# Optimization experiments

Measured on AMD Instinct MI355X. Metric: run time of the kernel, lower is better.

The kernel has to match this reference:

```python
import jax, jax.numpy as jnp
import numpy as np

B, T, D, V = 64, 2048, 64, 100000


def create_beta_stack(feats, times):
    """feats: [F,B,T] float, times: [B,T] float.
    beta[:, :, i] = (times[:,i]-times[:,i-1] + mask_{i-1} * beta[:,:,i-1]) * (times[:,i] != -1)
    where mask = (feat != -1) & (feat != 0). Sequential reset/accumulate scan over T."""
    dt = times[:, 1:] - times[:, :-1]                                   # [B, T-1]
    mask = ((feats[:, :, :-1] != -1) & (feats[:, :, :-1] != 0)).astype(feats.dtype)  # [F,B,T-1]
    pad = (times[:, 1:] != -1).astype(feats.dtype)                      # [B, T-1]

    def step(b, xs):
        dt_i, m_i, p_i = xs                      # [B], [F,B], [B]
        b_new = (dt_i[None, :] + m_i * b) * p_i[None, :]
        return b_new, b_new

    init = jnp.zeros(feats.shape[:2], feats.dtype)                      # [F,B]
    _, betas = jax.lax.scan(step, init, (dt.T, jnp.moveaxis(mask, 2, 0), pad.T))  # [T-1,F,B]
    beta = jnp.concatenate([init[None], betas], axis=0)                 # [T,F,B]
    return jnp.moveaxis(beta, 0, 2)                                     # [F,B,T]


def setup_inputs() -> dict:
    key = jax.random.key(0)
    ks = jax.random.split(key, 11)
    cat1 = jax.random.randint(ks[0], (B, T), 0, V)
    cat2 = jax.random.randint(ks[1], (B, T), 0, V)
    num1 = jax.random.normal(ks[2], (B, T), jnp.float32)
    num2 = jax.random.normal(ks[3], (B, T), jnp.float32)
    # integer-valued, sorted per row (event timestamps); no -1 padding
    event_time = jnp.sort(jax.random.randint(ks[4], (B, T), 0, 10000), axis=1).astype(jnp.float32)
    E1 = jax.random.normal(ks[5], (V, D), jnp.float32) * 0.02
    E2 = jax.random.normal(ks[6], (V, D), jnp.float32) * 0.02
    w1 = jax.random.normal(ks[7], (D,), jnp.float32) * 0.02
    b1 = jax.random.normal(ks[8], (D,), jnp.float32) * 0.02
    w2 = jax.random.normal(ks[9], (D,), jnp.float32) * 0.02
    b2 = jax.random.normal(ks[10], (D,), jnp.float32) * 0.02
    return {"cat1": cat1, "cat2": cat2, "num1": num1, "num2": num2,
            "event_time": event_time, "E1": E1, "E2": E2,
            "w1": w1, "b1": b1, "w2": w2, "b2": b2}


def reference(cat1, cat2, num1, num2, event_time, E1, E2, w1, b1, w2, b2):
    times = event_time.astype(jnp.float32)
    # categorical embeddings [B,T,D]
    emb1 = E1[cat1]
    emb2 = E2[cat2]
    # numeric Linear(1, D): values[...,None] @ W.T + b
    nemb1 = num1[..., None] * w1 + b1
    nemb2 = num2[..., None] * w2 + b2
    # time-since-last-valid-event recurrence, stacked over all 4 features
    feats = jnp.stack([cat1.astype(jnp.float32), cat2.astype(jnp.float32), num1, num2], axis=0)  # [4,B,T]
    betas = create_beta_stack(feats, times)                             # [4,B,T]
    rep = lambda x: jnp.broadcast_to(x[..., None], x.shape + (D,))
    delta = jnp.concatenate([rep(betas[0]), rep(betas[1]), rep(betas[2]), rep(betas[3])], axis=-1)  # [B,T,4D]
    m = lambda v: rep((v != -1) & (v != 0))
    mask = jnp.concatenate([m(cat1), m(cat2), m(num1), m(num2)], axis=-1)  # [B,T,4D] bool
    features = jnp.concatenate([emb1, emb2, nemb1, nemb2], axis=-1)     # [B,T,4D]
    return (features, times, delta, mask)
```

## Files before the change

kernel.cpp:

```cpp
#include <hip/hip_runtime.h>

#define BB 64
#define TT 2048
#define DD 64
#define BT (BB * TT)
#define OFF_F 0
#define OFF_T (BT * 256)
#define OFF_D (OFF_T + BT)
#define OFF_M (OFF_D + BT * 256)

__device__ __forceinline__ int pidx(int i) { return i + (i >> 5); }

__global__ __launch_bounds__(256) void beta_scan_kernel(
    const int* __restrict__ cat1, const int* __restrict__ cat2,
    const float* __restrict__ num1, const float* __restrict__ num2,
    const float* __restrict__ times, float* __restrict__ beta_ws)
{
    __shared__ float s_t[2112];
    __shared__ float s_f[4][2112];
    const int b   = blockIdx.x;
    const int tid = threadIdx.x;

    for (int i = tid; i < TT; i += 256) {
        int g = b * TT + i;
        s_t[pidx(i)]    = times[g];
        s_f[0][pidx(i)] = (float)cat1[g];
        s_f[1][pidx(i)] = (float)cat2[g];
        s_f[2][pidx(i)] = num1[g];
        s_f[3][pidx(i)] = num2[g];
    }
    __syncthreads();

    const int f    = tid >> 6;
    const int lane = tid & 63;
    const int lo   = lane * 32;

    float A = 1.f, C = 0.f;
    #pragma unroll
    for (int k = 0; k < 32; ++k) {
        int i = lo + k;
        float a, c;
        if (i == 0) { a = 0.f; c = 0.f; }
        else {
            float ti  = s_t[pidx(i)];
            float tp  = s_t[pidx(i - 1)];
            float fv  = s_f[f][pidx(i - 1)];
            float pad = (ti != -1.f) ? 1.f : 0.f;
            float m   = (fv != -1.f && fv != 0.f) ? 1.f : 0.f;
            a = m * pad;
            c = (ti - tp) * pad;
        }
        C = a * C + c;
        A = A * a;
    }
    for (int d = 1; d < 64; d <<= 1) {
        float Ap = __shfl_up(A, d);
        float Cp = __shfl_up(C, d);
        if (lane >= d) { C = A * Cp + C; A = A * Ap; }
    }
    float beta = __shfl_up(C, 1);
    if (lane == 0) beta = 0.f;

    float* out = beta_ws + (f * BB + b) * TT;
    #pragma unroll
    for (int k = 0; k < 32; ++k) {
        int i = lo + k;
        float a, c;
        if (i == 0) { a = 0.f; c = 0.f; }
        else {
            float ti  = s_t[pidx(i)];
            float tp  = s_t[pidx(i - 1)];
            float fv  = s_f[f][pidx(i - 1)];
            float pad = (ti != -1.f) ? 1.f : 0.f;
            float m   = (fv != -1.f && fv != 0.f) ? 1.f : 0.f;
            a = m * pad;
            c = (ti - tp) * pad;
        }
        beta = a * beta + c;
        out[i] = beta;
    }
}

__global__ __launch_bounds__(256) void expand_kernel(
    const int* __restrict__ cat1, const int* __restrict__ cat2,
    const float* __restrict__ num1, const float* __restrict__ num2,
    const float* __restrict__ times,
    const float* __restrict__ E1, const float* __restrict__ E2,
    const float* __restrict__ w1, const float* __restrict__ b1,
    const float* __restrict__ w2, const float* __restrict__ b2,
    const float* __restrict__ beta_ws, float* __restrict__ out)
{
    const int u  = blockIdx.x * 256 + threadIdx.x;
    const int f  = u >> 21;
    const int r  = u & ((1 << 21) - 1);
    const int bt = r >> 4;
    const int c  = r & 15;

    float4 v;
    float  mval;
    if (f == 0) {
        int idx = cat1[bt];
        v = ((const float4*)(E1 + (size_t)idx * DD))[c];
        mval = (idx != -1 && idx != 0) ? 1.f : 0.f;
    } else if (f == 1) {
        int idx = cat2[bt];
        v = ((const float4*)(E2 + (size_t)idx * DD))[c];
        mval = (idx != -1 && idx != 0) ? 1.f : 0.f;
    } else if (f == 2) {
        float x   = num1[bt];
        float4 w  = ((const float4*)w1)[c];
        float4 bb = ((const float4*)b1)[c];
        v = make_float4(x * w.x + bb.x, x * w.y + bb.y,
                        x * w.z + bb.z, x * w.w + bb.w);
        mval = (x != -1.f && x != 0.f) ? 1.f : 0.f;
    } else {
        float x   = num2[bt];
        float4 w  = ((const float4*)w2)[c];
        float4 bb = ((const float4*)b2)[c];
        v = make_float4(x * w.x + bb.x, x * w.y + bb.y,
                        x * w.z + bb.z, x * w.w + bb.w);
        mval = (x != -1.f && x != 0.f) ? 1.f : 0.f;
    }

    const float bv = beta_ws[f * BT + bt];
    const int widx = bt * 64 + f * 16 + c;

    ((float4*)(out + OFF_F))[widx] = v;
    ((float4*)(out + OFF_D))[widx] = make_float4(bv, bv, bv, bv);
    ((float4*)(out + OFF_M))[widx] = make_float4(mval, mval, mval, mval);

    if (u < BT / 4) {
        ((float4*)(out + OFF_T))[u] = ((const float4*)times)[u];
    }
}

extern "C" void kernel_launch(void* const* d_in, const int* in_sizes, int n_in,
                              void* d_out, int out_size, void* d_ws, size_t ws_size,
                              hipStream_t stream) {
    const int*   cat1  = (const int*)d_in[0];
    const int*   cat2  = (const int*)d_in[1];
    const float* num1  = (const float*)d_in[2];
    const float* num2  = (const float*)d_in[3];
    const float* times = (const float*)d_in[4];
    const float* E1    = (const float*)d_in[5];
    const float* E2    = (const float*)d_in[6];
    const float* w1    = (const float*)d_in[7];
    const float* b1    = (const float*)d_in[8];
    const float* w2    = (const float*)d_in[9];
    const float* b2    = (const float*)d_in[10];
    float* out     = (float*)d_out;
    float* beta_ws = (float*)d_ws;

    beta_scan_kernel<<<BB, 256, 0, stream>>>(cat1, cat2, num1, num2, times, beta_ws);

    const int nthreads = 4 * BT * 16;
    expand_kernel<<<nthreads / 256, 256, 0, stream>>>(
        cat1, cat2, num1, num2, times, E1, E2, w1, b1, w2, b2, beta_ws, out);
}
```

Measured before the change: 469.8 us.

## Split beta scan per feature, interleave beta workspace, fuse features in expand with nontemporal stores

The beta scan now runs one 64-thread block per (feature, batch) pair, which gives more blocks, and loads inputs with vector loads. The beta workspace is interleaved as [B,T,4] so the expand kernel can read all four betas with one float4 load. Each expand thread now handles all four features for one (bt, chunk) pair instead of one feature, which removes divergent branching and redundant index loads. All large output writes use nontemporal stores to avoid cache pollution. In exchange, the scan writes its workspace with stride 4, which is uncoalesced, and each expand thread has fewer blocks and more registers in flight.

Result: no change. 466.0 us (-0.8%).

```diff
diff --git a/kernel.cpp b/kernel.cpp
--- a/kernel.cpp
+++ b/kernel.cpp
@@ -9,31 +9,57 @@
 #define OFF_D (OFF_T + BT)
 #define OFF_M (OFF_D + BT * 256)
 
+typedef float v4f __attribute__((ext_vector_type(4)));
+
+__device__ __forceinline__ void nt_store4(float* p, float x, float y, float z, float w) {
+    v4f v = {x, y, z, w};
+    __builtin_nontemporal_store(v, (v4f*)p);
+}
+__device__ __forceinline__ void nt_store4v(float* p, float4 v) {
+    nt_store4(p, v.x, v.y, v.z, v.w);
+}
+
 __device__ __forceinline__ int pidx(int i) { return i + (i >> 5); }
 
-__global__ __launch_bounds__(256) void beta_scan_kernel(
+__global__ __launch_bounds__(64) void beta_scan_kernel(
     const int* __restrict__ cat1, const int* __restrict__ cat2,
     const float* __restrict__ num1, const float* __restrict__ num2,
     const float* __restrict__ times, float* __restrict__ beta_ws)
 {
     __shared__ float s_t[2112];
-    __shared__ float s_f[4][2112];
-    const int b   = blockIdx.x;
-    const int tid = threadIdx.x;
+    __shared__ float s_v[2112];
+    const int f    = blockIdx.x >> 6;
+    const int b    = blockIdx.x & 63;
+    const int lane = threadIdx.x;
 
-    for (int i = tid; i < TT; i += 256) {
-        int g = b * TT + i;
-        s_t[pidx(i)]    = times[g];
-        s_f[0][pidx(i)] = (float)cat1[g];
-        s_f[1][pidx(i)] = (float)cat2[g];
-        s_f[2][pidx(i)] = num1[g];
-        s_f[3][pidx(i)] = num2[g];
+    const float4* tsrc = (const float4*)(times + b * TT);
+    for (int i4 = lane; i4 < TT / 4; i4 += 64) {
+        float4 t = tsrc[i4];
+        int base = i4 * 4;
+        s_t[pidx(base + 0)] = t.x;
+        s_t[pidx(base + 1)] = t.y;
+        s_t[pidx(base + 2)] = t.z;
+        s_t[pidx(base + 3)] = t.w;
+        float4 v;
+        if (f == 0) {
+            int4 ci = ((const int4*)(cat1 + b * TT))[i4];
+            v = make_float4((float)ci.x, (float)ci.y, (float)ci.z, (float)ci.w);
+        } else if (f == 1) {
+            int4 ci = ((const int4*)(cat2 + b * TT))[i4];
+            v = make_float4((float)ci.x, (float)ci.y, (float)ci.z, (float)ci.w);
+        } else if (f == 2) {
+            v = ((const float4*)(num1 + b * TT))[i4];
+        } else {
+            v = ((const float4*)(num2 + b * TT))[i4];
+        }
+        s_v[pidx(base + 0)] = v.x;
+        s_v[pidx(base + 1)] = v.y;
+        s_v[pidx(base + 2)] = v.z;
+        s_v[pidx(base + 3)] = v.w;
     }
     __syncthreads();
 
-    const int f    = tid >> 6;
-    const int lane = tid & 63;
-    const int lo   = lane * 32;
+    const int lo = lane * 32;
 
     float A = 1.f, C = 0.f;
     #pragma unroll
@@ -44,7 +70,7 @@
         else {
             float ti  = s_t[pidx(i)];
             float tp  = s_t[pidx(i - 1)];
-            float fv  = s_f[f][pidx(i - 1)];
+            float fv  = s_v[pidx(i - 1)];
             float pad = (ti != -1.f) ? 1.f : 0.f;
             float m   = (fv != -1.f && fv != 0.f) ? 1.f : 0.f;
             a = m * pad;
@@ -61,7 +87,7 @@
     float beta = __shfl_up(C, 1);
     if (lane == 0) beta = 0.f;
 
-    float* out = beta_ws + (f * BB + b) * TT;
+    float* out = beta_ws + (size_t)b * TT * 4 + f;
     #pragma unroll
     for (int k = 0; k < 32; ++k) {
         int i = lo + k;
@@ -70,14 +96,14 @@
         else {
             float ti  = s_t[pidx(i)];
             float tp  = s_t[pidx(i - 1)];
-            float fv  = s_f[f][pidx(i - 1)];
+            float fv  = s_v[pidx(i - 1)];
             float pad = (ti != -1.f) ? 1.f : 0.f;
             float m   = (fv != -1.f && fv != 0.f) ? 1.f : 0.f;
             a = m * pad;
             c = (ti - tp) * pad;
         }
         beta = a * beta + c;
-        out[i] = beta;
+        out[i * 4] = beta;
     }
 }
 
@@ -91,46 +117,55 @@
     const float* __restrict__ beta_ws, float* __restrict__ out)
 {
     const int u  = blockIdx.x * 256 + threadIdx.x;
-    const int f  = u >> 21;
-    const int r  = u & ((1 << 21) - 1);
-    const int bt = r >> 4;
-    const int c  = r & 15;
+    const int bt = u >> 4;
+    const int c  = u & 15;
 
-    float4 v;
-    float  mval;
-    if (f == 0) {
-        int idx = cat1[bt];
-        v = ((const float4*)(E1 + (size_t)idx * DD))[c];
-        mval = (idx != -1 && idx != 0) ? 1.f : 0.f;
-    } else if (f == 1) {
-        int idx = cat2[bt];
-        v = ((const float4*)(E2 + (size_t)idx * DD))[c];
-        mval = (idx != -1 && idx != 0) ? 1.f : 0.f;
-    } else if (f == 2) {
-        float x   = num1[bt];
-        float4 w  = ((const float4*)w1)[c];
-        float4 bb = ((const float4*)b1)[c];
-        v = make_float4(x * w.x + bb.x, x * w.y + bb.y,
-                        x * w.z + bb.z, x * w.w + bb.w);
-        mval = (x != -1.f && x != 0.f) ? 1.f : 0.f;
-    } else {
-        float x   = num2[bt];
-        float4 w  = ((const float4*)w2)[c];
-        float4 bb = ((const float4*)b2)[c];
-        v = make_float4(x * w.x + bb.x, x * w.y + bb.y,
-                        x * w.z + bb.z, x * w.w + bb.w);
-        mval = (x != -1.f && x != 0.f) ? 1.f : 0.f;
-    }
+    const int   i1 = cat1[bt];
+    const int   i2 = cat2[bt];
+    const float x1 = num1[bt];
+    const float x2 = num2[bt];
 
-    const float bv = beta_ws[f * BT + bt];
-    const int widx = bt * 64 + f * 16 + c;
+    const float4 e1  = ((const float4*)(E1 + (size_t)i1 * DD))[c];
+    const float4 e2  = ((const float4*)(E2 + (size_t)i2 * DD))[c];
+    const float4 wc1 = ((const float4*)w1)[c];
+    const float4 bc1 = ((const float4*)b1)[c];
+    const float4 wc2 = ((const float4*)w2)[c];
+    const float4 bc2 = ((const float4*)b2)[c];
+    const float4 n1  = make_float4(x1 * wc1.x + bc1.x, x1 * wc1.y + bc1.y,
+                                   x1 * wc1.z + bc1.z, x1 * wc1.w + bc1.w);
+    const float4 n2  = make_float4(x2 * wc2.x + bc2.x, x2 * wc2.y + bc2.y,
+                                   x2 * wc2.z + bc2.z, x2 * wc2.w + bc2.w);
 
-    ((float4*)(out + OFF_F))[widx] = v;
-    ((float4*)(out + OFF_D))[widx] = make_float4(bv, bv, bv, bv);
-    ((float4*)(out + OFF_M))[widx] = make_float4(mval, mval, mval, mval);
+    const float4 bet = ((const float4*)beta_ws)[bt];
+
+    const float m1 = (i1 != -1 && i1 != 0) ? 1.f : 0.f;
+    const float m2 = (i2 != -1 && i2 != 0) ? 1.f : 0.f;
+    const float m3 = (x1 != -1.f && x1 != 0.f) ? 1.f : 0.f;
+    const float m4 = (x2 != -1.f && x2 != 0.f) ? 1.f : 0.f;
+
+    const int base = bt * 64 + c;
+    float* outF = out + OFF_F;
+    float* outD = out + OFF_D;
+    float* outM = out + OFF_M;
+
+    nt_store4v(outF + 4 * (base),      e1);
+    nt_store4v(outF + 4 * (base + 16), e2);
+    nt_store4v(outF + 4 * (base + 32), n1);
+    nt_store4v(outF + 4 * (base + 48), n2);
+
+    nt_store4(outD + 4 * (base),      bet.x, bet.x, bet.x, bet.x);
+    nt_store4(outD + 4 * (base + 16), bet.y, bet.y, bet.y, bet.y);
+    nt_store4(outD + 4 * (base + 32), bet.z, bet.z, bet.z, bet.z);
+    nt_store4(outD + 4 * (base + 48), bet.w, bet.w, bet.w, bet.w);
+
+    nt_store4(outM + 4 * (base),      m1, m1, m1, m1);
+    nt_store4(outM + 4 * (base + 16), m2, m2, m2, m2);
+    nt_store4(outM + 4 * (base + 32), m3, m3, m3, m3);
+    nt_store4(outM + 4 * (base + 48), m4, m4, m4, m4);
 
     if (u < BT / 4) {
-        ((float4*)(out + OFF_T))[u] = ((const float4*)times)[u];
+        float4 t = ((const float4*)times)[u];
+        nt_store4v(out + OFF_T + 4 * u, t);
     }
 }
 
@@ -151,9 +186,8 @@
     float* out     = (float*)d_out;
     float* beta_ws = (float*)d_ws;
 
-    beta_scan_kernel<<<BB, 256, 0, stream>>>(cat1, cat2, num1, num2, times, beta_ws);
+    beta_scan_kernel<<<4 * BB, 64, 0, stream>>>(cat1, cat2, num1, num2, times, beta_ws);
 
-    const int nthreads = 4 * BT * 16;
-    expand_kernel<<<nthreads / 256, 256, 0, stream>>>(
+    expand_kernel<<<(BT * 16) / 256, 256, 0, stream>>>(
         cat1, cat2, num1, num2, times, E1, E2, w1, b1, w2, b2, beta_ws, out);
 }
```
